# Performance work log

Hardware: AMD Instinct MI355X
Metric: run time of the kernel (lower is better)

## Reference

```python
import jax, jax.numpy as jnp
import numpy as np

HEADS = 8
DIM_HEAD = 64
DIM = 512
EPS = 1e-7  # module's self.eps, also used as LayerNorm eps


def _per_head_layernorm(t, w, b):
    # t: [b, h, n, d]; w, b: [h, d] (one LayerNorm per head, affine)
    mu = t.mean(axis=-1, keepdims=True)
    var = t.var(axis=-1, keepdims=True)  # biased, matches torch LayerNorm
    tn = (t - mu) * jax.lax.rsqrt(var + EPS)
    return tn * w[None, :, None, :] + b[None, :, None, :]


def setup_inputs() -> dict:
    key = jax.random.key(0)
    ks = jax.random.split(key, 4)
    inner = HEADS * DIM_HEAD
    return {
        "x": jax.random.normal(ks[0], (2, 2048, DIM), dtype=jnp.float32),
        "w_qkv": jax.random.normal(ks[1], (3 * inner, DIM), dtype=jnp.float32) * 0.02,
        "lnk_w": jnp.ones((HEADS, DIM_HEAD), dtype=jnp.float32),
        "lnk_b": jnp.zeros((HEADS, DIM_HEAD), dtype=jnp.float32),
        "lnv_w": jnp.ones((HEADS, DIM_HEAD), dtype=jnp.float32),
        "lnv_b": jnp.zeros((HEADS, DIM_HEAD), dtype=jnp.float32),
        "w_out": jax.random.normal(ks[2], (DIM, inner), dtype=jnp.float32) * 0.02,
        "b_out": jnp.zeros((DIM,), dtype=jnp.float32),
    }


def reference(x, w_qkv, lnk_w, lnk_b, lnv_w, lnv_b, w_out, b_out):
    b, n, _ = x.shape
    qkv = x @ w_qkv.T  # [b, n, 3*inner]
    q, k, v = jnp.split(qkv, 3, axis=-1)

    def split_heads(t):  # [b, n, h*d] -> [b, h, n, d]
        return t.reshape(b, n, HEADS, DIM_HEAD).transpose(0, 2, 1, 3)

    q, k, v = map(split_heads, (q, k, v))

    # per-head LayerNorm over dim_head on k and v
    k = _per_head_layernorm(k, lnk_w, lnk_b)
    v = _per_head_layernorm(v, lnv_w, lnv_b)

    # causal linear attention: prefix sums of k and of k-v outer products
    k_cum = jnp.cumsum(k, axis=2)  # [b, h, n, d]
    # scores: [b, h, n, d, e] prefix sums of outer products, scaled by 1/seq_len
    scores = jnp.cumsum(jnp.einsum('bhnd,bhne->bhnde', k, v), axis=2) / n
    d_inv = 1.0 / jnp.einsum('bhnd,bhnd->bhn', k_cum + EPS, q)  # [b, h, n]
    out = jnp.einsum('bhnd,bhnde,bhn->bhne', q, scores, d_inv)  # [b, h, n, e]

    out = out.transpose(0, 2, 1, 3).reshape(b, n, HEADS * DIM_HEAD)  # b n (h e)
    return out @ w_out.T + b_out
```

## Files before the change

### kernel.cpp

```cpp
#include <hip/hip_runtime.h>

constexpr int Bb   = 2;
constexpr int Nn   = 2048;
constexpr int Hh   = 8;
constexpr int Dd   = 64;
constexpr int Mm   = Bb * Nn;
constexpr int TQKV = 1536;
constexpr int INNER = Hh * Dd;
constexpr int CH   = 64;
constexpr int NCH  = Nn / CH;
constexpr int CSZ  = Dd * Dd + Dd;
constexpr float EPSF = 1e-7f;

typedef _Float16 half8 __attribute__((ext_vector_type(8)));
typedef _Float16 half4 __attribute__((ext_vector_type(4)));
typedef float f32x4 __attribute__((ext_vector_type(4)));

#define AS1(p) ((const __attribute__((address_space(1))) unsigned int*)(p))
#define AS3(p) ((__attribute__((address_space(3))) unsigned int*)(p))

__global__ __launch_bounds__(256) void gemm1_f32(
    const float* __restrict__ A, const float* __restrict__ B,
    float* __restrict__ C) {
  __shared__ float As[32][132];
  __shared__ float Bs[32][68];
  const int tid = threadIdx.x;
  const int tx = tid & 15, ty = tid >> 4;
  const int bm = blockIdx.y * 128, bn = blockIdx.x * 64;
  const int rowA = tid & 127, c4a = tid >> 7;
  const int rowB = tid & 63,  c4b = tid >> 6;

  float acc[8][4] = {};

  for (int k0 = 0; k0 < 512; k0 += 32) {
#pragma unroll
    for (int p = 0; p < 4; ++p) {
      int c4 = c4a + 2 * p;
      float4 fa = *(const float4*)(A + (size_t)(bm + rowA) * 512 + k0 + c4 * 4);
      As[c4 * 4 + 0][rowA] = fa.x; As[c4 * 4 + 1][rowA] = fa.y;
      As[c4 * 4 + 2][rowA] = fa.z; As[c4 * 4 + 3][rowA] = fa.w;
    }
#pragma unroll
    for (int p = 0; p < 2; ++p) {
      int c4 = c4b + 4 * p;
      float4 fb = *(const float4*)(B + (size_t)(bn + rowB) * 512 + k0 + c4 * 4);
      Bs[c4 * 4 + 0][rowB] = fb.x; Bs[c4 * 4 + 1][rowB] = fb.y;
      Bs[c4 * 4 + 2][rowB] = fb.z; Bs[c4 * 4 + 3][rowB] = fb.w;
    }
    __syncthreads();
#pragma unroll
    for (int kk = 0; kk < 32; ++kk) {
      float a[8], b[4];
      *(float4*)&a[0] = *(const float4*)&As[kk][ty * 8];
      *(float4*)&a[4] = *(const float4*)&As[kk][ty * 8 + 4];
      *(float4*)&b[0] = *(const float4*)&Bs[kk][tx * 4];
#pragma unroll
      for (int i = 0; i < 8; ++i)
#pragma unroll
        for (int j = 0; j < 4; ++j) acc[i][j] += a[i] * b[j];
    }
    __syncthreads();
  }

#pragma unroll
  for (int i = 0; i < 8; ++i) {
    size_t row = bm + ty * 8 + i;
    float4 r;
    r.x = acc[i][0]; r.y = acc[i][1]; r.z = acc[i][2]; r.w = acc[i][3];
    *(float4*)(C + row * (size_t)TQKV + bn + tx * 4) = r;
  }
}

__global__ __launch_bounds__(256) void split_f16_k(
    const float* __restrict__ s, _Float16* __restrict__ hi,
    _Float16* __restrict__ lo, int n4) {
  int i = blockIdx.x * 256 + threadIdx.x;
  if (i >= n4) return;
  float4 a = ((const float4*)s)[i];
  half4 h, l;
  float av[4] = {a.x, a.y, a.z, a.w};
#pragma unroll
  for (int j = 0; j < 4; ++j) {
    _Float16 hh = (_Float16)av[j];
    h[j] = hh;
    l[j] = (_Float16)((av[j] - (float)hh) * 2048.0f);
  }
  ((half4*)hi)[i] = h;
  ((half4*)lo)[i] = l;
}

__global__ __launch_bounds__(256) void gemm_split_nt(
    const _Float16* __restrict__ Ah, const _Float16* __restrict__ Al,
    const _Float16* __restrict__ Bh, const _Float16* __restrict__ Bl,
    const float* __restrict__ bias, float* __restrict__ C,
    int Ndim, int Kd) {
  constexpr int BM = 128, BN = 64, BK = 32;
  __shared__ _Float16 lds[(2 * BM + 2 * BN) * BK];
  constexpr int AHo = 0;
  constexpr int ALo = BM * BK;
  constexpr int BHo = 2 * BM * BK;
  constexpr int BLo = 2 * BM * BK + BN * BK;

  const int tid = threadIdx.x;
  const int wave = tid >> 6, lane = tid & 63;
  const int lq = lane >> 4, lm = lane & 15;
  const int bm = blockIdx.y * BM, bn = blockIdx.x * BN;

  f32x4 acc[2][4] = {};
  f32x4 corr[2][4] = {};

  const int nsteps = Kd >> 5;
  for (int ks = 0; ks < nsteps; ++ks) {
    const int k0 = ks * BK;
    for (int idx = wave; idx < 24; idx += 4) {
      int t, j;
      if (idx < 8)       { t = 0; j = idx; }
      else if (idx < 16) { t = 1; j = idx - 8; }
      else if (idx < 20) { t = 2; j = idx - 16; }
      else               { t = 3; j = idx - 20; }
      const int row = j * 16 + (lane >> 2);
      const _Float16* g;
      _Float16* l;
      if (t == 0)      { g = Ah + (size_t)(bm + row) * Kd; l = lds + AHo + j * 16 * BK; }
      else if (t == 1) { g = Al + (size_t)(bm + row) * Kd; l = lds + ALo + j * 16 * BK; }
      else if (t == 2) { g = Bh + (size_t)(bn + row) * Kd; l = lds + BHo + j * 16 * BK; }
      else             { g = Bl + (size_t)(bn + row) * Kd; l = lds + BLo + j * 16 * BK; }
      g += k0 + (lane & 3) * 8;
      __builtin_amdgcn_global_load_lds(AS1(g), AS3(l), 16, 0, 0);
    }
    __syncthreads();

    half8 ahf[2], alf[2], bhf[4], blf[4];
    const int mwo = wave * 32;
#pragma unroll
    for (int fi = 0; fi < 2; ++fi) {
      ahf[fi] = *(const half8*)&lds[AHo + (mwo + fi * 16 + lm) * BK + lq * 8];
      alf[fi] = *(const half8*)&lds[ALo + (mwo + fi * 16 + lm) * BK + lq * 8];
    }
#pragma unroll
    for (int fj = 0; fj < 4; ++fj) {
      bhf[fj] = *(const half8*)&lds[BHo + (fj * 16 + lm) * BK + lq * 8];
      blf[fj] = *(const half8*)&lds[BLo + (fj * 16 + lm) * BK + lq * 8];
    }
#pragma unroll
    for (int fi = 0; fi < 2; ++fi)
#pragma unroll
      for (int fj = 0; fj < 4; ++fj) {
        acc[fi][fj] = __builtin_amdgcn_mfma_f32_16x16x32_f16(
            ahf[fi], bhf[fj], acc[fi][fj], 0, 0, 0);
        corr[fi][fj] = __builtin_amdgcn_mfma_f32_16x16x32_f16(
            ahf[fi], blf[fj], corr[fi][fj], 0, 0, 0);
        corr[fi][fj] = __builtin_amdgcn_mfma_f32_16x16x32_f16(
            alf[fi], bhf[fj], corr[fi][fj], 0, 0, 0);
      }
    __syncthreads();
  }

#pragma unroll
  for (int fi = 0; fi < 2; ++fi) {
    const int m0 = bm + wave * 32 + fi * 16 + lq * 4;
#pragma unroll
    for (int fj = 0; fj < 4; ++fj) {
      const int n = bn + fj * 16 + lm;
      const float bb = bias ? bias[n] : 0.f;
      f32x4 v = acc[fi][fj];
      f32x4 cv = corr[fi][fj];
#pragma unroll
      for (int r = 0; r < 4; ++r)
        C[(size_t)(m0 + r) * Ndim + n] = v[r] + cv[r] * (1.0f / 2048.0f) + bb;
    }
  }
}

__global__ __launch_bounds__(256) void ln_kv(
    float* __restrict__ qkv,
    const float* __restrict__ lnk_w, const float* __restrict__ lnk_b,
    const float* __restrict__ lnv_w, const float* __restrict__ lnv_b) {
  int wave = (blockIdx.x * 256 + threadIdx.x) >> 6;
  int lane = threadIdx.x & 63;
  const int total = Bb * Nn * Hh;
  bool isv = wave >= total;
  int r = isv ? wave - total : wave;
  int bn = r / Hh, h = r % Hh;
  float* p = qkv + (size_t)bn * TQKV + (isv ? 2 * INNER : INNER) + h * Dd + lane;
  float val = *p;
  float s = val, s2 = val * val;
#pragma unroll
  for (int off = 32; off; off >>= 1) {
    s += __shfl_xor(s, off, 64);
    s2 += __shfl_xor(s2, off, 64);
  }
  float mean = s * (1.f / 64.f);
  float var = s2 * (1.f / 64.f) - mean * mean;
  float inv = 1.0f / sqrtf(var + EPSF);
  const float* w = isv ? lnv_w : lnk_w;
  const float* b = isv ? lnv_b : lnk_b;
  *p = (val - mean) * inv * w[h * Dd + lane] + b[h * Dd + lane];
}

__global__ __launch_bounds__(256) void chunk_sums(
    const float* __restrict__ qkv, float* __restrict__ cbuf) {
  int blk = blockIdx.x;
  int c = blk % NCH;
  int bh = blk / NCH;
  int h = bh % Hh, b = bh / Hh;
  __shared__ float Ks[CH][68];
  __shared__ float Vs[CH][68];
  int tid = threadIdx.x;
  const float* base = qkv + (size_t)(b * Nn + c * CH) * TQKV + h * Dd;
  for (int i = tid; i < CH * 16; i += 256) {
    int row = i >> 4, c4 = i & 15;
    *(float4*)&Ks[row][c4 * 4] =
        *(const float4*)(base + (size_t)row * TQKV + INNER + c4 * 4);
    *(float4*)&Vs[row][c4 * 4] =
        *(const float4*)(base + (size_t)row * TQKV + 2 * INNER + c4 * 4);
  }
  __syncthreads();
  int d0 = (tid >> 4) * 4, e0 = (tid & 15) * 4;
  float acc[4][4] = {};
  float kc[4] = {0.f, 0.f, 0.f, 0.f};
  for (int n = 0; n < CH; ++n) {
    float4 kv = *(const float4*)&Ks[n][d0];
    float4 vv = *(const float4*)&Vs[n][e0];
    float ka[4] = {kv.x, kv.y, kv.z, kv.w};
    float va[4] = {vv.x, vv.y, vv.z, vv.w};
#pragma unroll
    for (int i = 0; i < 4; ++i)
#pragma unroll
      for (int j = 0; j < 4; ++j) acc[i][j] += ka[i] * va[j];
    if (e0 == 0) {
#pragma unroll
      for (int i = 0; i < 4; ++i) kc[i] += ka[i];
    }
  }
  float* out = cbuf + (size_t)blk * CSZ;
#pragma unroll
  for (int i = 0; i < 4; ++i) {
    float4 r;
    r.x = acc[i][0]; r.y = acc[i][1]; r.z = acc[i][2]; r.w = acc[i][3];
    *(float4*)(out + (size_t)(d0 + i) * Dd + e0) = r;
  }
  if (e0 == 0) {
#pragma unroll
    for (int i = 0; i < 4; ++i) out[Dd * Dd + d0 + i] = kc[i];
  }
}

__global__ __launch_bounds__(256) void chunk_prefix(float* __restrict__ cbuf) {
  int bh = blockIdx.y;
  int i = blockIdx.x * 256 + threadIdx.x;
  if (i >= CSZ) return;
  float* p = cbuf + (size_t)bh * NCH * CSZ + i;
  float carry = 0.f;
  for (int c = 0; c < NCH; ++c) {
    float t = p[(size_t)c * CSZ];
    p[(size_t)c * CSZ] = carry;
    carry += t;
  }
}

__global__ __launch_bounds__(256) void chunk_attn(
    const float* __restrict__ qkv, const float* __restrict__ cbuf,
    _Float16* __restrict__ atth, _Float16* __restrict__ attl) {
  int blk = blockIdx.x;
  int c = blk % NCH;
  int bh = blk / NCH;
  int h = bh % Hh, b = bh / Hh;
  __shared__ float Qs[64][68];
  __shared__ float Ks[64][68];
  __shared__ float Vs[64][68];
  __shared__ float Ps[64][68];
  __shared__ float Ss[64][68];
  __shared__ float kcs[64];
  __shared__ float rs[64][17];
  __shared__ float denomS[64];

  int tid = threadIdx.x;
  int tx = tid & 15, ty = tid >> 4;
  const float* base = qkv + (size_t)(b * Nn + c * CH) * TQKV + h * Dd;
  for (int i = tid; i < CH * 16; i += 256) {
    int row = i >> 4, c4 = i & 15;
    float4 fq = *(const float4*)(base + (size_t)row * TQKV + c4 * 4);
    Qs[c4 * 4 + 0][row] = fq.x; Qs[c4 * 4 + 1][row] = fq.y;
    Qs[c4 * 4 + 2][row] = fq.z; Qs[c4 * 4 + 3][row] = fq.w;
    float4 fk = *(const float4*)(base + (size_t)row * TQKV + INNER + c4 * 4);
    Ks[c4 * 4 + 0][row] = fk.x; Ks[c4 * 4 + 1][row] = fk.y;
    Ks[c4 * 4 + 2][row] = fk.z; Ks[c4 * 4 + 3][row] = fk.w;
    float4 fv = *(const float4*)(base + (size_t)row * TQKV + 2 * INNER + c4 * 4);
    *(float4*)&Vs[row][c4 * 4] = fv;
  }
  const float* sp = cbuf + (size_t)blk * CSZ;
  for (int i = tid; i < 1024; i += 256) {
    int row = i >> 4;
    *(float4*)&Ss[row][(i & 15) * 4] = *(const float4*)(sp + (size_t)i * 4);
  }
  if (tid < 16) {
    float4 f = *(const float4*)(sp + Dd * Dd + tid * 4);
    kcs[tid * 4 + 0] = f.x; kcs[tid * 4 + 1] = f.y;
    kcs[tid * 4 + 2] = f.z; kcs[tid * 4 + 3] = f.w;
  }
  __syncthreads();

  float accP[4][4] = {};
  for (int kk = 0; kk < 64; ++kk) {
    float4 qa = *(const float4*)&Qs[kk][ty * 4];
    float4 kb = *(const float4*)&Ks[kk][tx * 4];
    float qv[4] = {qa.x, qa.y, qa.z, qa.w};
    float kv[4] = {kb.x, kb.y, kb.z, kb.w};
#pragma unroll
    for (int i = 0; i < 4; ++i)
#pragma unroll
      for (int j = 0; j < 4; ++j) accP[i][j] += qv[i] * kv[j];
  }
#pragma unroll
  for (int i = 0; i < 4; ++i) {
    int n = ty * 4 + i;
    float rsum = 0.f;
#pragma unroll
    for (int j = 0; j < 4; ++j) {
      int m = tx * 4 + j;
      float p = (m <= n) ? accP[i][j] : 0.f;
      Ps[m][n] = p;
      rsum += p;
    }
    rs[n][tx] = rsum;
  }
  __syncthreads();

  float accO[4][4] = {};
  for (int d = 0; d < 64; ++d) {
    float4 qa = *(const float4*)&Qs[d][ty * 4];
    float4 sb = *(const float4*)&Ss[d][tx * 4];
    float qv[4] = {qa.x, qa.y, qa.z, qa.w};
    float sv[4] = {sb.x, sb.y, sb.z, sb.w};
#pragma unroll
    for (int i = 0; i < 4; ++i)
#pragma unroll
      for (int j = 0; j < 4; ++j) accO[i][j] += qv[i] * sv[j];
  }
  if (tid < 64) {
    int n = tid;
    float qkc = 0.f, qs = 0.f;
    for (int d = 0; d < 64; ++d) {
      float q = Qs[d][n];
      qkc += q * kcs[d];
      qs += q;
    }
    float rsum = 0.f;
#pragma unroll
    for (int t2 = 0; t2 < 16; ++t2) rsum += rs[n][t2];
    denomS[n] = qkc + rsum + EPSF * qs;
  }
  __syncthreads();

  for (int m = 0; m < 64; ++m) {
    float4 pa = *(const float4*)&Ps[m][ty * 4];
    float4 vb = *(const float4*)&Vs[m][tx * 4];
    float pv[4] = {pa.x, pa.y, pa.z, pa.w};
    float vv[4] = {vb.x, vb.y, vb.z, vb.w};
#pragma unroll
    for (int i = 0; i < 4; ++i)
#pragma unroll
      for (int j = 0; j < 4; ++j) accO[i][j] += pv[i] * vv[j];
  }

  size_t obase = (size_t)(b * Nn + c * CH) * INNER + h * Dd;
#pragma unroll
  for (int i = 0; i < 4; ++i) {
    int n = ty * 4 + i;
    float dinv = 1.0f / denomS[n];
    float scale = dinv * (1.0f / (float)Nn);
    half4 hv, lv;
#pragma unroll
    for (int j = 0; j < 4; ++j) {
      float o = accO[i][j] * scale;
      _Float16 hh = (_Float16)o;
      hv[j] = hh;
      lv[j] = (_Float16)((o - (float)hh) * 2048.0f);
    }
    *(half4*)(atth + obase + (size_t)n * INNER + tx * 4) = hv;
    *(half4*)(attl + obase + (size_t)n * INNER + tx * 4) = lv;
  }
}

extern "C" void kernel_launch(void* const* d_in, const int* in_sizes, int n_in,
                              void* d_out, int out_size, void* d_ws,
                              size_t ws_size, hipStream_t stream) {
  const float* x     = (const float*)d_in[0];
  const float* w_qkv = (const float*)d_in[1];
  const float* lnk_w = (const float*)d_in[2];
  const float* lnk_b = (const float*)d_in[3];
  const float* lnv_w = (const float*)d_in[4];
  const float* lnv_b = (const float*)d_in[5];
  const float* w_out = (const float*)d_in[6];
  const float* b_out = (const float*)d_in[7];
  float* out = (float*)d_out;

  float* qkv  = (float*)d_ws;
  float* cbuf = qkv + (size_t)Mm * TQKV;
  _Float16* atth = (_Float16*)(cbuf + (size_t)Bb * Hh * NCH * CSZ);
  _Float16* attl = atth + (size_t)Mm * INNER;
  _Float16* woh  = attl + (size_t)Mm * INNER;
  _Float16* wol  = woh + (size_t)INNER * 512;

  gemm1_f32<<<dim3(TQKV / 64, Mm / 128), 256, 0, stream>>>(x, w_qkv, qkv);

  ln_kv<<<(2 * Bb * Nn * Hh * 64) / 256, 256, 0, stream>>>(
      qkv, lnk_w, lnk_b, lnv_w, lnv_b);

  chunk_sums<<<Bb * Hh * NCH, 256, 0, stream>>>(qkv, cbuf);

  chunk_prefix<<<dim3((CSZ + 255) / 256, Bb * Hh), 256, 0, stream>>>(cbuf);

  split_f16_k<<<256, 256, 0, stream>>>(w_out, woh, wol, INNER * 512 / 4);

  chunk_attn<<<Bb * Hh * NCH, 256, 0, stream>>>(qkv, cbuf, atth, attl);

  gemm_split_nt<<<dim3(INNER / 64, Mm / 128), 256, 0, stream>>>(
      atth, attl, woh, wol, b_out, out, INNER, 512);
}
```

Baseline: 237.4 us.

## Fuse K/V LayerNorm into chunk sums, shrink QKV GEMM tile, alias P buffer

Removes the standalone ln_kv kernel and applies the per-head LayerNorm inside chunk_sums on the shared-memory K/V tiles, then writes the normalized values back to the qkv buffer for chunk_attn. The QKV GEMM changes from 128x64 tiles with 256 threads to 64x64 tiles with 128 threads, doubling the block count. chunk_attn reuses the K tile's shared memory for P, which needs an extra barrier, and cuts shared memory use. Together these save one launch and one pass over K/V in global memory. The cost is a serial per-row normalization in which only 128 threads do the work.

Measured after the change: 238.2 us. About the same (+0.3%).

```diff
diff --git a/kernel.cpp b/kernel.cpp
--- a/kernel.cpp
+++ b/kernel.cpp
@@ -19,33 +19,28 @@
 #define AS1(p) ((const __attribute__((address_space(1))) unsigned int*)(p))
 #define AS3(p) ((__attribute__((address_space(3))) unsigned int*)(p))
 
-__global__ __launch_bounds__(256) void gemm1_f32(
+__global__ __launch_bounds__(128) void gemm1_f32(
     const float* __restrict__ A, const float* __restrict__ B,
     float* __restrict__ C) {
-  __shared__ float As[32][132];
+  __shared__ float As[32][68];
   __shared__ float Bs[32][68];
   const int tid = threadIdx.x;
   const int tx = tid & 15, ty = tid >> 4;
-  const int bm = blockIdx.y * 128, bn = blockIdx.x * 64;
-  const int rowA = tid & 127, c4a = tid >> 7;
-  const int rowB = tid & 63,  c4b = tid >> 6;
+  const int bm = blockIdx.y * 64, bn = blockIdx.x * 64;
+  const int row = tid & 63, c4base = tid >> 6;
 
   float acc[8][4] = {};
 
   for (int k0 = 0; k0 < 512; k0 += 32) {
 #pragma unroll
     for (int p = 0; p < 4; ++p) {
-      int c4 = c4a + 2 * p;
-      float4 fa = *(const float4*)(A + (size_t)(bm + rowA) * 512 + k0 + c4 * 4);
-      As[c4 * 4 + 0][rowA] = fa.x; As[c4 * 4 + 1][rowA] = fa.y;
-      As[c4 * 4 + 2][rowA] = fa.z; As[c4 * 4 + 3][rowA] = fa.w;
-    }
-#pragma unroll
-    for (int p = 0; p < 2; ++p) {
-      int c4 = c4b + 4 * p;
-      float4 fb = *(const float4*)(B + (size_t)(bn + rowB) * 512 + k0 + c4 * 4);
-      Bs[c4 * 4 + 0][rowB] = fb.x; Bs[c4 * 4 + 1][rowB] = fb.y;
-      Bs[c4 * 4 + 2][rowB] = fb.z; Bs[c4 * 4 + 3][rowB] = fb.w;
+      int c4 = c4base + 2 * p;
+      float4 fa = *(const float4*)(A + (size_t)(bm + row) * 512 + k0 + c4 * 4);
+      As[c4 * 4 + 0][row] = fa.x; As[c4 * 4 + 1][row] = fa.y;
+      As[c4 * 4 + 2][row] = fa.z; As[c4 * 4 + 3][row] = fa.w;
+      float4 fb = *(const float4*)(B + (size_t)(bn + row) * 512 + k0 + c4 * 4);
+      Bs[c4 * 4 + 0][row] = fb.x; Bs[c4 * 4 + 1][row] = fb.y;
+      Bs[c4 * 4 + 2][row] = fb.z; Bs[c4 * 4 + 3][row] = fb.w;
     }
     __syncthreads();
 #pragma unroll
@@ -64,10 +59,10 @@
 
 #pragma unroll
   for (int i = 0; i < 8; ++i) {
-    size_t row = bm + ty * 8 + i;
-    float4 r;
-    r.x = acc[i][0]; r.y = acc[i][1]; r.z = acc[i][2]; r.w = acc[i][3];
-    *(float4*)(C + row * (size_t)TQKV + bn + tx * 4) = r;
+    size_t r = bm + ty * 8 + i;
+    float4 v;
+    v.x = acc[i][0]; v.y = acc[i][1]; v.z = acc[i][2]; v.w = acc[i][3];
+    *(float4*)(C + r * (size_t)TQKV + bn + tx * 4) = v;
   }
 }
 
@@ -172,34 +167,10 @@
   }
 }
 
-__global__ __launch_bounds__(256) void ln_kv(
-    float* __restrict__ qkv,
-    const float* __restrict__ lnk_w, const float* __restrict__ lnk_b,
-    const float* __restrict__ lnv_w, const float* __restrict__ lnv_b) {
-  int wave = (blockIdx.x * 256 + threadIdx.x) >> 6;
-  int lane = threadIdx.x & 63;
-  const int total = Bb * Nn * Hh;
-  bool isv = wave >= total;
-  int r = isv ? wave - total : wave;
-  int bn = r / Hh, h = r % Hh;
-  float* p = qkv + (size_t)bn * TQKV + (isv ? 2 * INNER : INNER) + h * Dd + lane;
-  float val = *p;
-  float s = val, s2 = val * val;
-#pragma unroll
-  for (int off = 32; off; off >>= 1) {
-    s += __shfl_xor(s, off, 64);
-    s2 += __shfl_xor(s2, off, 64);
-  }
-  float mean = s * (1.f / 64.f);
-  float var = s2 * (1.f / 64.f) - mean * mean;
-  float inv = 1.0f / sqrtf(var + EPSF);
-  const float* w = isv ? lnv_w : lnk_w;
-  const float* b = isv ? lnv_b : lnk_b;
-  *p = (val - mean) * inv * w[h * Dd + lane] + b[h * Dd + lane];
-}
-
-__global__ __launch_bounds__(256) void chunk_sums(
-    const float* __restrict__ qkv, float* __restrict__ cbuf) {
+__global__ __launch_bounds__(256) void chunk_sums_ln(
+    float* __restrict__ qkv, const float* __restrict__ lnk_w,
+    const float* __restrict__ lnk_b, const float* __restrict__ lnv_w,
+    const float* __restrict__ lnv_b, float* __restrict__ cbuf) {
   int blk = blockIdx.x;
   int c = blk % NCH;
   int bh = blk / NCH;
@@ -207,7 +178,7 @@
   __shared__ float Ks[CH][68];
   __shared__ float Vs[CH][68];
   int tid = threadIdx.x;
-  const float* base = qkv + (size_t)(b * Nn + c * CH) * TQKV + h * Dd;
+  float* base = qkv + (size_t)(b * Nn + c * CH) * TQKV + h * Dd;
   for (int i = tid; i < CH * 16; i += 256) {
     int row = i >> 4, c4 = i & 15;
     *(float4*)&Ks[row][c4 * 4] =
@@ -216,6 +187,37 @@
         *(const float4*)(base + (size_t)row * TQKV + 2 * INNER + c4 * 4);
   }
   __syncthreads();
+
+  if (tid < 128) {
+    bool isv = tid >= 64;
+    int row = tid & 63;
+    float* R = isv ? &Vs[row][0] : &Ks[row][0];
+    float s = 0.f, s2 = 0.f;
+#pragma unroll
+    for (int j = 0; j < 64; j += 4) {
+      float4 v = *(const float4*)&R[j];
+      s += v.x + v.y + v.z + v.w;
+      s2 += v.x * v.x + v.y * v.y + v.z * v.z + v.w * v.w;
+    }
+    float mean = s * (1.f / 64.f);
+    float var = s2 * (1.f / 64.f) - mean * mean;
+    float inv = 1.0f / sqrtf(var + EPSF);
+    const float* w = isv ? lnv_w : lnk_w;
+    const float* bb = isv ? lnv_b : lnk_b;
+#pragma unroll
+    for (int j = 0; j < 64; ++j)
+      R[j] = (R[j] - mean) * inv * w[h * Dd + j] + bb[h * Dd + j];
+  }
+  __syncthreads();
+
+  for (int i = tid; i < CH * 16; i += 256) {
+    int row = i >> 4, c4 = i & 15;
+    *(float4*)(base + (size_t)row * TQKV + INNER + c4 * 4) =
+        *(const float4*)&Ks[row][c4 * 4];
+    *(float4*)(base + (size_t)row * TQKV + 2 * INNER + c4 * 4) =
+        *(const float4*)&Vs[row][c4 * 4];
+  }
+
   int d0 = (tid >> 4) * 4, e0 = (tid & 15) * 4;
   float acc[4][4] = {};
   float kc[4] = {0.f, 0.f, 0.f, 0.f};
@@ -269,11 +271,11 @@
   __shared__ float Qs[64][68];
   __shared__ float Ks[64][68];
   __shared__ float Vs[64][68];
-  __shared__ float Ps[64][68];
   __shared__ float Ss[64][68];
   __shared__ float kcs[64];
   __shared__ float rs[64][17];
   __shared__ float denomS[64];
+  float (*Ps)[68] = Ks;
 
   int tid = threadIdx.x;
   int tx = tid & 15, ty = tid >> 4;
@@ -312,6 +314,8 @@
 #pragma unroll
       for (int j = 0; j < 4; ++j) accP[i][j] += qv[i] * kv[j];
   }
+  __syncthreads();
+
 #pragma unroll
   for (int i = 0; i < 4; ++i) {
     int n = ty * 4 + i;
@@ -403,12 +407,10 @@
   _Float16* woh  = attl + (size_t)Mm * INNER;
   _Float16* wol  = woh + (size_t)INNER * 512;
 
-  gemm1_f32<<<dim3(TQKV / 64, Mm / 128), 256, 0, stream>>>(x, w_qkv, qkv);
-
-  ln_kv<<<(2 * Bb * Nn * Hh * 64) / 256, 256, 0, stream>>>(
-      qkv, lnk_w, lnk_b, lnv_w, lnv_b);
-
-  chunk_sums<<<Bb * Hh * NCH, 256, 0, stream>>>(qkv, cbuf);
+  gemm1_f32<<<dim3(TQKV / 64, Mm / 64), 128, 0, stream>>>(x, w_qkv, qkv);
+
+  chunk_sums_ln<<<Bb * Hh * NCH, 256, 0, stream>>>(
+      qkv, lnk_w, lnk_b, lnv_w, lnv_b, cbuf);
 
   chunk_prefix<<<dim3((CSZ + 255) / 256, Bb * Hh), 256, 0, stream>>>(cbuf);
 
```
